# Optimization experiments

Measured on AMD Instinct MI355X. Metric: run time of the kernel, lower is better.

The kernel has to match this reference:

```python
import jax, jax.numpy as jnp
import numpy as np

B, D, L, N, M, K = 256, 512, 196, 1024, 512, 10000  # batch, context, num_ctx, hidden, embed, vocab


def setup_inputs() -> dict:
    key = jax.random.key(0)
    ks = jax.random.split(key, 20)
    r = lambda k, s: jax.random.normal(k, s, dtype=jnp.float32) * 0.02
    return {
        "a_i": jax.random.normal(ks[0], (B, D, L), dtype=jnp.float32),
        "inp": jax.random.normal(ks[1], (B, 1, K), dtype=jnp.float32),
        "hn_prev": jax.random.normal(ks[2], (B, 1, N), dtype=jnp.float32),
        "cn_prev": jax.random.normal(ks[3], (B, 1, N), dtype=jnp.float32),
        "f_att_w": r(ks[4], (N + D,)),  # Linear(n+D -> 1), stored as a vector
        "f_att_b": r(ks[5], (1,)),
        "gate_w": r(ks[6], (N,)),       # Linear(n -> 1)
        "gate_b": r(ks[7], (1,)),
        "E_w": r(ks[8], (M, K)),        # torch Linear weight [out, in]
        "E_b": r(ks[9], (M,)),
        "W_ih": r(ks[10], (4 * N, D + N + M)),  # LSTM input->hidden (i,f,g,o)
        "W_hh": r(ks[11], (4 * N, N)),
        "b_ih": r(ks[12], (4 * N,)),
        "b_hh": r(ks[13], (4 * N,)),
        "Lh_w": r(ks[14], (M, N)),
        "Lh_b": r(ks[15], (M,)),
        "Lz_w": r(ks[16], (M, D)),
        "Lz_b": r(ks[17], (M,)),
        "Lo_w": r(ks[18], (K, M)),
        "Lo_b": r(ks[19], (K,)),
    }


def reference(a_i, inp, hn_prev, cn_prev,
              f_att_w, f_att_b, gate_w, gate_b,
              E_w, E_b, W_ih, W_hh, b_ih, b_hh,
              Lh_w, Lh_b, Lz_w, Lz_b, Lo_w, Lo_b):
    h = hn_prev[:, 0]  # [B, N]
    c = cn_prev[:, 0]  # [B, N]
    # --- additive attention: the 196-iteration torch loop batched into one einsum ---
    # cat((a_i[:,:,i], h)) @ f_att_w splits into the a-part and h-part of the weight.
    w_a, w_h = f_att_w[:D], f_att_w[D:]
    e = jnp.einsum('bdl,d->bl', a_i, w_a) + (h @ w_h)[:, None] + f_att_b  # [B, L]
    alpha = jax.nn.softmax(e, axis=1)                                     # [B, L]
    beta = jax.nn.sigmoid(h @ gate_w + gate_b)                            # [B]
    z = beta[:, None] * jnp.einsum('bl,bdl->bd', alpha, a_i)              # [B, D]
    # --- word embedding ---
    w_emb = inp[:, 0] @ E_w.T + E_b                                       # [B, M]
    # --- single-step LSTM (PyTorch gate order i, f, g, o) ---
    x = jnp.concatenate([w_emb, h, z], axis=1)                            # [B, M+N+D]
    gates = x @ W_ih.T + b_ih + h @ W_hh.T + b_hh                         # [B, 4N]
    i_g, f_g, g_g, o_g = jnp.split(gates, 4, axis=1)
    cn = jax.nn.sigmoid(f_g) * c + jax.nn.sigmoid(i_g) * jnp.tanh(g_g)
    hn = jax.nn.sigmoid(o_g) * jnp.tanh(cn)
    # --- output projection ---
    deep_out = w_emb + (hn @ Lh_w.T + Lh_b) + (z @ Lz_w.T + Lz_b)         # [B, M]
    p_yt = deep_out @ Lo_w.T + Lo_b                                       # [B, K]
    return (p_yt[:, None, :], hn[:, None, :], cn[:, None, :], alpha[:, None, :])
```

## Files before the change

kernel.cpp:

```cpp
#include <hip/hip_runtime.h>
#include <hip/hip_bf16.h>
#include <math.h>

#define BB 256
#define DD 512
#define LL 196
#define NN 1024
#define MM 512
#define KK 10000

#define OUT_PY 0
#define OUT_HN ((size_t)2560000)
#define OUT_CN ((size_t)2822144)
#define OUT_AL ((size_t)3084288)

#define OFF_PE    ((size_t)0)
#define OFF_BETA  ((size_t)401408)
#define OFF_Z     ((size_t)401664)
#define OFF_EMB   ((size_t)532736)
#define OFF_DEEP  ((size_t)663808)
#define OFF_EMBP  ((size_t)794880)
#define OFF_GATESP ((size_t)2892032)
#define OFF_DP    ((size_t)9183488)

typedef __attribute__((ext_vector_type(8))) short short8v;
typedef __attribute__((ext_vector_type(4))) float f32x4;

__device__ __forceinline__ short bfs(float f) {
    __hip_bfloat16 h = __float2bfloat16(f);
    return *reinterpret_cast<short*>(&h);
}

__device__ __forceinline__ short8v stage8(const float* __restrict__ p, bool ok,
                                          int kbase, int Ktot) {
    short8v v;
    if (ok && (kbase + 7 < Ktot)) {
        const float4 x = *(const float4*)(p + kbase);
        const float4 y = *(const float4*)(p + kbase + 4);
        v[0] = bfs(x.x); v[1] = bfs(x.y); v[2] = bfs(x.z); v[3] = bfs(x.w);
        v[4] = bfs(y.x); v[5] = bfs(y.y); v[6] = bfs(y.z); v[7] = bfs(y.w);
    } else {
#pragma unroll
        for (int i = 0; i < 8; ++i) {
            const int k = kbase + i;
            v[i] = bfs((ok && k < Ktot) ? p[k] : 0.f);
        }
    }
    return v;
}

struct GSrc { const float* A; int lda; const float* B; int ldb; int ktn; int K; };

__device__ __forceinline__ void gemm_body(
    const int bx, const int by, const int bz, const int rowBlocks,
    const GSrc s1, const GSrc s2,
    float* __restrict__ C, const int ldc, const int Ncols,
    const int ktPerSplit, const float* __restrict__ bias,
    short (*As)[64][72], short (*Bs)[64][72])
{
    const int t = threadIdx.x;
    const int row0 = bx * 64;
    const int col0 = by * 64;
    const int ktTot = s1.ktn + s2.ktn;
    const int kt0 = bz * ktPerSplit;
    const int nk = min(ktTot, kt0 + ktPerSplit) - kt0;

    const int sr = t >> 2;
    const int sk = (t & 3) << 4;
    const int bc = col0 + sr;
    const bool bok = (bc < Ncols);
    const float* aP1 = s1.A + (size_t)(row0 + sr) * s1.lda;
    const float* bP1 = s1.B + (size_t)(bok ? bc : 0) * s1.ldb;
    const float* aP2 = s2.A ? (s2.A + (size_t)(row0 + sr) * s2.lda) : aP1;
    const float* bP2 = s2.A ? (s2.B + (size_t)(bok ? bc : 0) * s2.ldb) : bP1;

    const int l = t & 63, w = t >> 6;
    const int wrow = (w >> 1) * 32, wcol = (w & 1) * 32;
    const int lr = l & 15, g = l >> 4, g8 = g * 8;

    f32x4 acc[2][2] = {};

    short8v sa0, sa1, sb0, sb1;
    {
        const int ktg = kt0;
        const float* aR; const float* bR; int kk, Kt;
        if (ktg < s1.ktn) { aR = aP1; bR = bP1; kk = (ktg << 6) + sk; Kt = s1.K; }
        else              { aR = aP2; bR = bP2; kk = ((ktg - s1.ktn) << 6) + sk; Kt = s2.K; }
        sa0 = stage8(aR, true, kk, Kt);  sa1 = stage8(aR, true, kk + 8, Kt);
        sb0 = stage8(bR, bok,  kk, Kt);  sb1 = stage8(bR, bok,  kk + 8, Kt);
    }
    *(short8v*)&As[0][sr][sk] = sa0; *(short8v*)&As[0][sr][sk + 8] = sa1;
    *(short8v*)&Bs[0][sr][sk] = sb0; *(short8v*)&Bs[0][sr][sk + 8] = sb1;
    __syncthreads();

    int cur = 0;
    for (int kt = 0; kt < nk; ++kt) {
        const bool more = (kt + 1 < nk);
        if (more) {
            const int ktg = kt0 + kt + 1;
            const float* aR; const float* bR; int kk, Kt;
            if (ktg < s1.ktn) { aR = aP1; bR = bP1; kk = (ktg << 6) + sk; Kt = s1.K; }
            else              { aR = aP2; bR = bP2; kk = ((ktg - s1.ktn) << 6) + sk; Kt = s2.K; }
            sa0 = stage8(aR, true, kk, Kt);  sa1 = stage8(aR, true, kk + 8, Kt);
            sb0 = stage8(bR, bok,  kk, Kt);  sb1 = stage8(bR, bok,  kk + 8, Kt);
        }
#pragma unroll
        for (int ks = 0; ks < 2; ++ks) {
            const int ko = ks * 32 + g8;
            short8v a0 = *(const short8v*)&As[cur][wrow + lr][ko];
            short8v a1 = *(const short8v*)&As[cur][wrow + 16 + lr][ko];
            short8v b0 = *(const short8v*)&Bs[cur][wcol + lr][ko];
            short8v b1 = *(const short8v*)&Bs[cur][wcol + 16 + lr][ko];
            acc[0][0] = __builtin_amdgcn_mfma_f32_16x16x32_bf16(a0, b0, acc[0][0], 0, 0, 0);
            acc[0][1] = __builtin_amdgcn_mfma_f32_16x16x32_bf16(a0, b1, acc[0][1], 0, 0, 0);
            acc[1][0] = __builtin_amdgcn_mfma_f32_16x16x32_bf16(a1, b0, acc[1][0], 0, 0, 0);
            acc[1][1] = __builtin_amdgcn_mfma_f32_16x16x32_bf16(a1, b1, acc[1][1], 0, 0, 0);
        }
        if (more) {
            *(short8v*)&As[cur ^ 1][sr][sk] = sa0;
            *(short8v*)&As[cur ^ 1][sr][sk + 8] = sa1;
            *(short8v*)&Bs[cur ^ 1][sr][sk] = sb0;
            *(short8v*)&Bs[cur ^ 1][sr][sk + 8] = sb1;
        }
        __syncthreads();
        cur ^= 1;
    }

    float* Cp = C + (size_t)bz * ((size_t)rowBlocks * 64) * ldc;
#pragma unroll
    for (int m = 0; m < 2; ++m)
#pragma unroll
        for (int n = 0; n < 2; ++n)
#pragma unroll
            for (int j = 0; j < 4; ++j) {
                const int r = row0 + wrow + m * 16 + g * 4 + j;
                const int c = col0 + wcol + n * 16 + lr;
                if (c < Ncols) {
                    float v = acc[m][n][j];
                    if (bias) v += bias[c];
                    Cp[(size_t)r * ldc + c] = v;
                }
            }
}

__global__ __launch_bounds__(256) void p1_atte_emb(
    const float* __restrict__ a_i, const float* __restrict__ f_att_w,
    float* __restrict__ pe,
    const float* __restrict__ inp, const float* __restrict__ E_w,
    float* __restrict__ embp)
{
    __shared__ __align__(16) short As[2][64][72];
    __shared__ __align__(16) short Bs[2][64][72];
    const int bid = blockIdx.x;
    if (bid < 2048) {
        const int b = bid >> 3, ch = bid & 7;
        const int l = threadIdx.x;
        if (l >= LL) return;
        const float* ap = a_i + ((size_t)b * DD + ch * 64) * LL + l;
        const float* wp = f_att_w + ch * 64;
        float s = 0.f;
#pragma unroll 16
        for (int d = 0; d < 64; ++d) s += ap[(size_t)d * LL] * wp[d];
        pe[((size_t)b * 8 + ch) * LL + l] = s;
    } else {
        const int i = bid - 2048;
        GSrc s1 = {inp, KK, E_w, KK, 157, KK};
        GSrc s2 = {nullptr, 0, nullptr, 0, 0, 0};
        gemm_body(i & 3, (i >> 2) & 7, i >> 5, 4, s1, s2,
                  embp, MM, MM, 10, nullptr, As, Bs);
    }
}

__global__ __launch_bounds__(256) void p2_softmax_embred(
    const float* __restrict__ pe, const float* __restrict__ h,
    const float* __restrict__ f_att_w, const float* __restrict__ f_att_b,
    const float* __restrict__ gate_w, const float* __restrict__ gate_b,
    float* __restrict__ alpha_out, float* __restrict__ beta,
    const float* __restrict__ embp, const float* __restrict__ E_b,
    float* __restrict__ emb)
{
    const int bid = blockIdx.x;
    const int t = threadIdx.x;
    if (bid < 256) {
        const int b = bid;
        __shared__ float red[256];
        __shared__ float red2[256];
        const float4 h4 = *(const float4*)(h + (size_t)b * NN + t * 4);
        const float4 w4 = *(const float4*)(f_att_w + DD + t * 4);
        const float4 g4 = *(const float4*)(gate_w + t * 4);
        float hd = h4.x * w4.x + h4.y * w4.y + h4.z * w4.z + h4.w * w4.w;
        float gd = h4.x * g4.x + h4.y * g4.y + h4.z * g4.z + h4.w * g4.w;
        red[t] = hd; red2[t] = gd;
        __syncthreads();
        for (int s = 128; s > 0; s >>= 1) {
            if (t < s) { red[t] += red[t + s]; red2[t] += red2[t + s]; }
            __syncthreads();
        }
        const float hdot = red[0];
        const float gdot = red2[0];
        __syncthreads();
        float e = -3.4e38f;
        if (t < LL) {
            const float* p = pe + (size_t)b * 8 * LL + t;
            e = hdot + f_att_b[0];
#pragma unroll
            for (int ch = 0; ch < 8; ++ch) e += p[ch * LL];
        }
        red[t] = e;
        __syncthreads();
        for (int s = 128; s > 0; s >>= 1) {
            if (t < s) red[t] = fmaxf(red[t], red[t + s]);
            __syncthreads();
        }
        const float mx = red[0];
        __syncthreads();
        const float ex = (t < LL) ? expf(e - mx) : 0.f;
        red[t] = ex;
        __syncthreads();
        for (int s = 128; s > 0; s >>= 1) {
            if (t < s) red[t] += red[t + s];
            __syncthreads();
        }
        const float inv = 1.f / red[0];
        if (t < LL) alpha_out[(size_t)b * LL + t] = ex * inv;
        if (t == 0) beta[b] = 1.f / (1.f + expf(-(gdot + gate_b[0])));
    } else {
        const int idx = (bid - 256) * 256 + t;
        const int j = idx & 511;
        float v = E_b[j];
#pragma unroll
        for (int s = 0; s < 16; ++s) v += embp[(size_t)s * (BB * 512) + idx];
        emb[idx] = v;
    }
}

__global__ __launch_bounds__(256) void p3_attz_gatesh(
    const float* __restrict__ a_i, const float* __restrict__ alpha,
    const float* __restrict__ beta, float* __restrict__ z,
    const float* __restrict__ h, const float* __restrict__ W_ih,
    const float* __restrict__ W_hh, float* __restrict__ gatesp)
{
    __shared__ __align__(16) short As[2][64][72];
    __shared__ __align__(16) short Bs[2][64][72];
    const int bid = blockIdx.x;
    if (bid < 8192) {
        const int b = bid >> 5, chunk = bid & 31;
        const int wave = threadIdx.x >> 6, lane = threadIdx.x & 63;
        const float* alp = alpha + (size_t)b * LL;
#pragma unroll
        for (int i = 0; i < 4; ++i) {
            const int d = chunk * 16 + wave * 4 + i;
            const float* ap = a_i + ((size_t)b * DD + d) * LL;
            float s = 0.f;
#pragma unroll
            for (int q = 0; q < 4; ++q) {
                const int lidx = lane + q * 64;
                if (lidx < LL) s += ap[lidx] * alp[lidx];
            }
#pragma unroll
            for (int off = 32; off > 0; off >>= 1) s += __shfl_down(s, off, 64);
            if (lane == 0) z[(size_t)b * DD + d] = beta[b] * s;
        }
    } else {
        const int i = bid - 8192;
        GSrc s1 = {h, NN, W_ih + 512, 2048, 16, NN};
        GSrc s2 = {h, NN, W_hh, NN, 16, NN};
        gemm_body(i & 3, (i >> 2) & 63, i >> 8, 4, s1, s2,
                  gatesp, 4096, 4096, 8, nullptr, As, Bs);
    }
}

__global__ __launch_bounds__(256) void p4_gatesez_lz(
    const float* __restrict__ emb, const float* __restrict__ z,
    const float* __restrict__ W_ih, float* __restrict__ gatesp_hi,
    const float* __restrict__ Lz_w, float* __restrict__ dp)
{
    __shared__ __align__(16) short As[2][64][72];
    __shared__ __align__(16) short Bs[2][64][72];
    const int bid = blockIdx.x;
    if (bid < 512) {
        GSrc s1 = {emb, MM, W_ih, 2048, 8, MM};
        GSrc s2 = {z, DD, W_ih + 1536, 2048, 8, DD};
        gemm_body(bid & 3, (bid >> 2) & 63, bid >> 8, 4, s1, s2,
                  gatesp_hi, 4096, 4096, 8, nullptr, As, Bs);
    } else {
        const int i = bid - 512;
        GSrc s1 = {z, DD, Lz_w, DD, 8, DD};
        GSrc s2 = {nullptr, 0, nullptr, 0, 0, 0};
        gemm_body(i & 3, (i >> 2) & 7, i >> 5, 4, s1, s2,
                  dp, MM, MM, 1, nullptr, As, Bs);
    }
}

__global__ __launch_bounds__(256) void p5_lstm(
    const float* __restrict__ gatesp,
    const float* __restrict__ b_ih, const float* __restrict__ b_hh,
    const float* __restrict__ c_prev, float* __restrict__ hn, float* __restrict__ cn)
{
    const int idx = blockIdx.x * 256 + threadIdx.x;
    const int b = idx >> 10, n = idx & 1023;
    float g[4];
#pragma unroll
    for (int gi = 0; gi < 4; ++gi) {
        const int col = gi * 1024 + n;
        const size_t o = (size_t)b * 4096 + col;
        float v = b_ih[col] + b_hh[col];
#pragma unroll
        for (int s = 0; s < 6; ++s) v += gatesp[(size_t)s * (BB * 4096) + o];
        g[gi] = v;
    }
    const float si = 1.f / (1.f + expf(-g[0]));
    const float sf = 1.f / (1.f + expf(-g[1]));
    const float so = 1.f / (1.f + expf(-g[3]));
    const float tg = tanhf(g[2]);
    const float c = c_prev[idx];
    const float cnv = sf * c + si * tg;
    const float hnv = so * tanhf(cnv);
    cn[idx] = cnv;
    hn[idx] = hnv;
}

__global__ __launch_bounds__(256) void p6_lh(
    const float* __restrict__ hn, const float* __restrict__ Lh_w,
    float* __restrict__ dp_hi)
{
    __shared__ __align__(16) short As[2][64][72];
    __shared__ __align__(16) short Bs[2][64][72];
    const int bid = blockIdx.x;
    GSrc s1 = {hn, NN, Lh_w, NN, 16, NN};
    GSrc s2 = {nullptr, 0, nullptr, 0, 0, 0};
    gemm_body(bid & 3, (bid >> 2) & 7, bid >> 5, 4, s1, s2,
              dp_hi, MM, MM, 1, nullptr, As, Bs);
}

__global__ __launch_bounds__(256) void p7_deep(
    const float* __restrict__ emb, const float* __restrict__ dp,
    const float* __restrict__ Lh_b, const float* __restrict__ Lz_b,
    float* __restrict__ deep)
{
    const int idx = blockIdx.x * 256 + threadIdx.x;
    const int j = idx & 511;
    float v = emb[idx] + Lh_b[j] + Lz_b[j];
#pragma unroll
    for (int s = 0; s < 24; ++s) v += dp[(size_t)s * (BB * 512) + idx];
    deep[idx] = v;
}

__global__ __launch_bounds__(256) void p8_pyt(
    const float* __restrict__ deep, const float* __restrict__ Lo_w,
    const float* __restrict__ Lo_b, float* __restrict__ out)
{
    __shared__ __align__(16) short As[2][64][72];
    __shared__ __align__(16) short Bs[2][64][72];
    const int bid = blockIdx.x;
    GSrc s1 = {deep, MM, Lo_w, MM, 8, MM};
    GSrc s2 = {nullptr, 0, nullptr, 0, 0, 0};
    gemm_body(bid & 3, bid >> 2, 0, 4, s1, s2,
              out, KK, KK, 8, Lo_b, As, Bs);
}

extern "C" void kernel_launch(void* const* d_in, const int* in_sizes, int n_in,
                              void* d_out, int out_size, void* d_ws, size_t ws_size,
                              hipStream_t stream)
{
    const float* a_i     = (const float*)d_in[0];
    const float* inp     = (const float*)d_in[1];
    const float* hn_prev = (const float*)d_in[2];
    const float* cn_prev = (const float*)d_in[3];
    const float* f_att_w = (const float*)d_in[4];
    const float* f_att_b = (const float*)d_in[5];
    const float* gate_w  = (const float*)d_in[6];
    const float* gate_b  = (const float*)d_in[7];
    const float* E_w     = (const float*)d_in[8];
    const float* E_b     = (const float*)d_in[9];
    const float* W_ih    = (const float*)d_in[10];
    const float* W_hh    = (const float*)d_in[11];
    const float* b_ih    = (const float*)d_in[12];
    const float* b_hh    = (const float*)d_in[13];
    const float* Lh_w    = (const float*)d_in[14];
    const float* Lh_b    = (const float*)d_in[15];
    const float* Lz_w    = (const float*)d_in[16];
    const float* Lz_b    = (const float*)d_in[17];
    const float* Lo_w    = (const float*)d_in[18];
    const float* Lo_b    = (const float*)d_in[19];

    float* out = (float*)d_out;
    float* ws  = (float*)d_ws;

    float* PE     = ws + OFF_PE;
    float* BETA   = ws + OFF_BETA;
    float* Z      = ws + OFF_Z;
    float* EMB    = ws + OFF_EMB;
    float* DEEP   = ws + OFF_DEEP;
    float* EMBP   = ws + OFF_EMBP;
    float* GATESP = ws + OFF_GATESP;
    float* DP     = ws + OFF_DP;

    p1_atte_emb<<<2560, 256, 0, stream>>>(a_i, f_att_w, PE, inp, E_w, EMBP);

    p2_softmax_embred<<<768, 256, 0, stream>>>(PE, hn_prev, f_att_w, f_att_b,
                                               gate_w, gate_b, out + OUT_AL, BETA,
                                               EMBP, E_b, EMB);

    p3_attz_gatesh<<<9216, 256, 0, stream>>>(a_i, out + OUT_AL, BETA, Z,
                                             hn_prev, W_ih, W_hh, GATESP);

    p4_gatesez_lz<<<768, 256, 0, stream>>>(EMB, Z, W_ih,
                                           GATESP + (size_t)4 * BB * 4096,
                                           Lz_w, DP);

    p5_lstm<<<1024, 256, 0, stream>>>(GATESP, b_ih, b_hh, cn_prev,
                                      out + OUT_HN, out + OUT_CN);

    p6_lh<<<512, 256, 0, stream>>>(out + OUT_HN, Lh_w,
                                   DP + (size_t)8 * BB * 512);

    p7_deep<<<512, 256, 0, stream>>>(EMB, DP, Lh_b, Lz_b, DEEP);

    p8_pyt<<<628, 256, 0, stream>>>(DEEP, Lo_w, Lo_b, out + OUT_PY);
}
```

Measured before the change: 156.9 us.

## Fuse attention softmax and context into one register-resident pass over a_i

The attention score, softmax and context reduction are merged into one block per batch row. That block reads a_i once, packs it to bf16 in registers, transposes it through LDS for the score dot products, then reuses the registers for the alpha-weighted sum. This removes the separate partial-score buffer, the beta buffer and the second full read of a_i. The h-projection GEMM and embedding GEMM are co-scheduled in the same launch, with the embedding split-K halved (20 k-tiles per split), cutting kernel launches from 8 to 7. The cost is heavy register pressure (196 packed values per thread) and bf16 rounding of a_i in the attention math, which may spill or reduce accuracy.

```diff
diff --git a/kernel.cpp b/kernel.cpp
--- a/kernel.cpp
+++ b/kernel.cpp
@@ -14,21 +14,29 @@
 #define OUT_CN ((size_t)2822144)
 #define OUT_AL ((size_t)3084288)
 
-#define OFF_PE    ((size_t)0)
-#define OFF_BETA  ((size_t)401408)
-#define OFF_Z     ((size_t)401664)
-#define OFF_EMB   ((size_t)532736)
-#define OFF_DEEP  ((size_t)663808)
-#define OFF_EMBP  ((size_t)794880)
-#define OFF_GATESP ((size_t)2892032)
-#define OFF_DP    ((size_t)9183488)
+#define OFF_Z      ((size_t)0)
+#define OFF_EMB    ((size_t)131072)
+#define OFF_DEEP   ((size_t)262144)
+#define OFF_EMBP   ((size_t)393216)
+#define OFF_GATESP ((size_t)1441792)
+#define OFF_DP     ((size_t)7733248)
 
 typedef __attribute__((ext_vector_type(8))) short short8v;
 typedef __attribute__((ext_vector_type(4))) float f32x4;
 
-__device__ __forceinline__ short bfs(float f) {
-    __hip_bfloat16 h = __float2bfloat16(f);
-    return *reinterpret_cast<short*>(&h);
+__device__ __forceinline__ unsigned short f2bf(float f) {
+    unsigned int u = __builtin_bit_cast(unsigned int, f);
+    u += 0x7fffu + ((u >> 16) & 1u);
+    return (unsigned short)(u >> 16);
+}
+__device__ __forceinline__ unsigned int pk2(float a, float b) {
+    return ((unsigned int)f2bf(b) << 16) | (unsigned int)f2bf(a);
+}
+__device__ __forceinline__ float bflo(unsigned int u) {
+    return __builtin_bit_cast(float, u << 16);
+}
+__device__ __forceinline__ float bfhi(unsigned int u) {
+    return __builtin_bit_cast(float, u & 0xffff0000u);
 }
 
 __device__ __forceinline__ short8v stage8(const float* __restrict__ p, bool ok,
@@ -37,13 +45,15 @@
     if (ok && (kbase + 7 < Ktot)) {
         const float4 x = *(const float4*)(p + kbase);
         const float4 y = *(const float4*)(p + kbase + 4);
-        v[0] = bfs(x.x); v[1] = bfs(x.y); v[2] = bfs(x.z); v[3] = bfs(x.w);
-        v[4] = bfs(y.x); v[5] = bfs(y.y); v[6] = bfs(y.z); v[7] = bfs(y.w);
+        v[0] = (short)f2bf(x.x); v[1] = (short)f2bf(x.y);
+        v[2] = (short)f2bf(x.z); v[3] = (short)f2bf(x.w);
+        v[4] = (short)f2bf(y.x); v[5] = (short)f2bf(y.y);
+        v[6] = (short)f2bf(y.z); v[7] = (short)f2bf(y.w);
     } else {
 #pragma unroll
         for (int i = 0; i < 8; ++i) {
             const int k = kbase + i;
-            v[i] = bfs((ok && k < Ktot) ? p[k] : 0.f);
+            v[i] = (short)f2bf((ok && k < Ktot) ? p[k] : 0.f);
         }
     }
     return v;
@@ -143,126 +153,144 @@
             }
 }
 
-__global__ __launch_bounds__(256) void p1_atte_emb(
-    const float* __restrict__ a_i, const float* __restrict__ f_att_w,
-    float* __restrict__ pe,
-    const float* __restrict__ inp, const float* __restrict__ E_w,
-    float* __restrict__ embp)
-{
-    __shared__ __align__(16) short As[2][64][72];
-    __shared__ __align__(16) short Bs[2][64][72];
-    const int bid = blockIdx.x;
-    if (bid < 2048) {
-        const int b = bid >> 3, ch = bid & 7;
-        const int l = threadIdx.x;
-        if (l >= LL) return;
-        const float* ap = a_i + ((size_t)b * DD + ch * 64) * LL + l;
-        const float* wp = f_att_w + ch * 64;
-        float s = 0.f;
-#pragma unroll 16
-        for (int d = 0; d < 64; ++d) s += ap[(size_t)d * LL] * wp[d];
-        pe[((size_t)b * 8 + ch) * LL + l] = s;
-    } else {
-        const int i = bid - 2048;
-        GSrc s1 = {inp, KK, E_w, KK, 157, KK};
-        GSrc s2 = {nullptr, 0, nullptr, 0, 0, 0};
-        gemm_body(i & 3, (i >> 2) & 7, i >> 5, 4, s1, s2,
-                  embp, MM, MM, 10, nullptr, As, Bs);
-    }
-}
-
-__global__ __launch_bounds__(256) void p2_softmax_embred(
-    const float* __restrict__ pe, const float* __restrict__ h,
+__global__ __launch_bounds__(256, 2) void k1_att_emb_gatesh(
+    const float* __restrict__ a_i, const float* __restrict__ h,
     const float* __restrict__ f_att_w, const float* __restrict__ f_att_b,
     const float* __restrict__ gate_w, const float* __restrict__ gate_b,
-    float* __restrict__ alpha_out, float* __restrict__ beta,
-    const float* __restrict__ embp, const float* __restrict__ E_b,
-    float* __restrict__ emb)
-{
+    float* __restrict__ alpha_out, float* __restrict__ z,
+    const float* __restrict__ inp, const float* __restrict__ E_w,
+    float* __restrict__ embp,
+    const float* __restrict__ W_ih, const float* __restrict__ W_hh,
+    float* __restrict__ gatesp)
+{
+    __shared__ __align__(16) unsigned char smem[36864];
     const int bid = blockIdx.x;
     const int t = threadIdx.x;
+
     if (bid < 256) {
+        unsigned int* chunk = (unsigned int*)smem;
+        float* wsh = (float*)(smem + 26112);
+        float* al  = wsh + 512;
+        float* red = al + 200;
+        float* sc2 = red + 32;
+        const int lane = t & 63, w = t >> 6;
         const int b = bid;
-        __shared__ float red[256];
-        __shared__ float red2[256];
+
+        wsh[t] = f_att_w[t];
+        wsh[t + 256] = f_att_w[t + 256];
+
         const float4 h4 = *(const float4*)(h + (size_t)b * NN + t * 4);
         const float4 w4 = *(const float4*)(f_att_w + DD + t * 4);
         const float4 g4 = *(const float4*)(gate_w + t * 4);
         float hd = h4.x * w4.x + h4.y * w4.y + h4.z * w4.z + h4.w * w4.w;
         float gd = h4.x * g4.x + h4.y * g4.y + h4.z * g4.z + h4.w * g4.w;
-        red[t] = hd; red2[t] = gd;
-        __syncthreads();
-        for (int s = 128; s > 0; s >>= 1) {
-            if (t < s) { red[t] += red[t + s]; red2[t] += red2[t + s]; }
+#pragma unroll
+        for (int off = 32; off > 0; off >>= 1) {
+            hd += __shfl_down(hd, off, 64);
+            gd += __shfl_down(gd, off, 64);
+        }
+        if (lane == 0) { red[w] = hd; red[16 + w] = gd; }
+
+        unsigned int r0[98], r1[98];
+        const float* p0 = a_i + ((size_t)b * DD + t) * LL;
+        const float* p1 = p0 + (size_t)256 * LL;
+#pragma unroll
+        for (int j = 0; j < 49; ++j) {
+            const float4 v = *(const float4*)(p0 + j * 4);
+            r0[2 * j]     = pk2(v.x, v.y);
+            r0[2 * j + 1] = pk2(v.z, v.w);
+        }
+#pragma unroll
+        for (int j = 0; j < 49; ++j) {
+            const float4 v = *(const float4*)(p1 + j * 4);
+            r1[2 * j]     = pk2(v.x, v.y);
+            r1[2 * j + 1] = pk2(v.z, v.w);
+        }
+        __syncthreads();
+        if (t == 0) {
+            sc2[0] = red[0] + red[1] + red[2] + red[3];
+            sc2[1] = red[16] + red[17] + red[18] + red[19];
+        }
+
+        float e_acc = 0.f;
+#pragma unroll
+        for (int c = 0; c < 8; ++c) {
             __syncthreads();
-        }
-        const float hdot = red[0];
-        const float gdot = red2[0];
-        __syncthreads();
-        float e = -3.4e38f;
+            if (w == (c & 3)) {
+                unsigned int* dst = chunk + lane * 102;
+                if (c < 4) {
+#pragma unroll
+                    for (int j = 0; j < 49; ++j) {
+                        uint2 uv; uv.x = r0[2 * j]; uv.y = r0[2 * j + 1];
+                        *(uint2*)(dst + 2 * j) = uv;
+                    }
+                } else {
+#pragma unroll
+                    for (int j = 0; j < 49; ++j) {
+                        uint2 uv; uv.x = r1[2 * j]; uv.y = r1[2 * j + 1];
+                        *(uint2*)(dst + 2 * j) = uv;
+                    }
+                }
+            }
+            __syncthreads();
+            if (t < LL) {
+                const float* wc = wsh + c * 64;
+                const unsigned short* cs = (const unsigned short*)chunk;
+#pragma unroll
+                for (int d = 0; d < 64; ++d) {
+                    const float av = __builtin_bit_cast(
+                        float, (unsigned int)cs[d * 204 + t] << 16);
+                    e_acc += av * wc[d];
+                }
+            }
+        }
+        __syncthreads();
+
+        float e = (t < LL) ? (e_acc + sc2[0] + f_att_b[0]) : -3.4e38f;
+        float m = e;
+#pragma unroll
+        for (int off = 32; off > 0; off >>= 1) m = fmaxf(m, __shfl_down(m, off, 64));
+        if (lane == 0) red[w] = m;
+        __syncthreads();
+        const float mx = fmaxf(fmaxf(red[0], red[1]), fmaxf(red[2], red[3]));
+        const float ex = (t < LL) ? expf(e - mx) : 0.f;
+        float s = ex;
+#pragma unroll
+        for (int off = 32; off > 0; off >>= 1) s += __shfl_down(s, off, 64);
+        if (lane == 0) red[16 + w] = s;
+        __syncthreads();
+        const float inv = 1.f / (red[16] + red[17] + red[18] + red[19]);
         if (t < LL) {
-            const float* p = pe + (size_t)b * 8 * LL + t;
-            e = hdot + f_att_b[0];
-#pragma unroll
-            for (int ch = 0; ch < 8; ++ch) e += p[ch * LL];
-        }
-        red[t] = e;
-        __syncthreads();
-        for (int s = 128; s > 0; s >>= 1) {
-            if (t < s) red[t] = fmaxf(red[t], red[t + s]);
-            __syncthreads();
-        }
-        const float mx = red[0];
-        __syncthreads();
-        const float ex = (t < LL) ? expf(e - mx) : 0.f;
-        red[t] = ex;
-        __syncthreads();
-        for (int s = 128; s > 0; s >>= 1) {
-            if (t < s) red[t] += red[t + s];
-            __syncthreads();
-        }
-        const float inv = 1.f / red[0];
-        if (t < LL) alpha_out[(size_t)b * LL + t] = ex * inv;
-        if (t == 0) beta[b] = 1.f / (1.f + expf(-(gdot + gate_b[0])));
+            const float a = ex * inv;
+            al[t] = a;
+            alpha_out[(size_t)b * LL + t] = a;
+        }
+        __syncthreads();
+
+        float d0 = 0.f, d1 = 0.f;
+#pragma unroll
+        for (int j = 0; j < 49; ++j) {
+            const float4 a4 = *(const float4*)(al + 4 * j);
+            d0 += bflo(r0[2 * j]) * a4.x + bfhi(r0[2 * j]) * a4.y
+                + bflo(r0[2 * j + 1]) * a4.z + bfhi(r0[2 * j + 1]) * a4.w;
+            d1 += bflo(r1[2 * j]) * a4.x + bfhi(r1[2 * j]) * a4.y
+                + bflo(r1[2 * j + 1]) * a4.z + bfhi(r1[2 * j + 1]) * a4.w;
+        }
+        const float beta = 1.f / (1.f + expf(-(sc2[1] + gate_b[0])));
+        z[(size_t)b * DD + t] = beta * d0;
+        z[(size_t)b * DD + 256 + t] = beta * d1;
+    } else if (bid < 512) {
+        short (*As)[64][72] = (short (*)[64][72])smem;
+        short (*Bs)[64][72] = (short (*)[64][72])(smem + 18432);
+        const int i = bid - 256;
+        GSrc s1 = {inp, KK, E_w, KK, 157, KK};
+        GSrc s2 = {nullptr, 0, nullptr, 0, 0, 0};
+        gemm_body(i & 3, (i >> 2) & 7, i >> 5, 4, s1, s2,
+                  embp, MM, MM, 20, nullptr, As, Bs);
     } else {
-        const int idx = (bid - 256) * 256 + t;
-        const int j = idx & 511;
-        float v = E_b[j];
-#pragma unroll
-        for (int s = 0; s < 16; ++s) v += embp[(size_t)s * (BB * 512) + idx];
-        emb[idx] = v;
-    }
-}
-
-__global__ __launch_bounds__(256) void p3_attz_gatesh(
-    const float* __restrict__ a_i, const float* __restrict__ alpha,
-    const float* __restrict__ beta, float* __restrict__ z,
-    const float* __restrict__ h, const float* __restrict__ W_ih,
-    const float* __restrict__ W_hh, float* __restrict__ gatesp)
-{
-    __shared__ __align__(16) short As[2][64][72];
-    __shared__ __align__(16) short Bs[2][64][72];
-    const int bid = blockIdx.x;
-    if (bid < 8192) {
-        const int b = bid >> 5, chunk = bid & 31;
-        const int wave = threadIdx.x >> 6, lane = threadIdx.x & 63;
-        const float* alp = alpha + (size_t)b * LL;
-#pragma unroll
-        for (int i = 0; i < 4; ++i) {
-            const int d = chunk * 16 + wave * 4 + i;
-            const float* ap = a_i + ((size_t)b * DD + d) * LL;
-            float s = 0.f;
-#pragma unroll
-            for (int q = 0; q < 4; ++q) {
-                const int lidx = lane + q * 64;
-                if (lidx < LL) s += ap[lidx] * alp[lidx];
-            }
-#pragma unroll
-            for (int off = 32; off > 0; off >>= 1) s += __shfl_down(s, off, 64);
-            if (lane == 0) z[(size_t)b * DD + d] = beta[b] * s;
-        }
-    } else {
-        const int i = bid - 8192;
+        short (*As)[64][72] = (short (*)[64][72])smem;
+        short (*Bs)[64][72] = (short (*)[64][72])(smem + 18432);
+        const int i = bid - 512;
         GSrc s1 = {h, NN, W_ih + 512, 2048, 16, NN};
         GSrc s2 = {h, NN, W_hh, NN, 16, NN};
         gemm_body(i & 3, (i >> 2) & 63, i >> 8, 4, s1, s2,
@@ -270,13 +298,26 @@
     }
 }
 
-__global__ __launch_bounds__(256) void p4_gatesez_lz(
+__global__ __launch_bounds__(256) void k2_embred(
+    const float* __restrict__ embp, const float* __restrict__ E_b,
+    float* __restrict__ emb)
+{
+    const int idx = blockIdx.x * 256 + threadIdx.x;
+    const int j = idx & 511;
+    float v = E_b[j];
+#pragma unroll
+    for (int s = 0; s < 8; ++s) v += embp[(size_t)s * (BB * 512) + idx];
+    emb[idx] = v;
+}
+
+__global__ __launch_bounds__(256) void k3_gatesez_lz(
     const float* __restrict__ emb, const float* __restrict__ z,
     const float* __restrict__ W_ih, float* __restrict__ gatesp_hi,
     const float* __restrict__ Lz_w, float* __restrict__ dp)
 {
-    __shared__ __align__(16) short As[2][64][72];
-    __shared__ __align__(16) short Bs[2][64][72];
+    __shared__ __align__(16) unsigned char smem[36864];
+    short (*As)[64][72] = (short (*)[64][72])smem;
+    short (*Bs)[64][72] = (short (*)[64][72])(smem + 18432);
     const int bid = blockIdx.x;
     if (bid < 512) {
         GSrc s1 = {emb, MM, W_ih, 2048, 8, MM};
@@ -292,7 +333,7 @@
     }
 }
 
-__global__ __launch_bounds__(256) void p5_lstm(
+__global__ __launch_bounds__(256) void k4_lstm(
     const float* __restrict__ gatesp,
     const float* __restrict__ b_ih, const float* __restrict__ b_hh,
     const float* __restrict__ c_prev, float* __restrict__ hn, float* __restrict__ cn)
@@ -320,12 +361,13 @@
     hn[idx] = hnv;
 }
 
-__global__ __launch_bounds__(256) void p6_lh(
+__global__ __launch_bounds__(256) void k5_lh(
     const float* __restrict__ hn, const float* __restrict__ Lh_w,
     float* __restrict__ dp_hi)
 {
-    __shared__ __align__(16) short As[2][64][72];
-    __shared__ __align__(16) short Bs[2][64][72];
+    __shared__ __align__(16) unsigned char smem[36864];
+    short (*As)[64][72] = (short (*)[64][72])smem;
+    short (*Bs)[64][72] = (short (*)[64][72])(smem + 18432);
     const int bid = blockIdx.x;
     GSrc s1 = {hn, NN, Lh_w, NN, 16, NN};
     GSrc s2 = {nullptr, 0, nullptr, 0, 0, 0};
@@ -333,7 +375,7 @@
               dp_hi, MM, MM, 1, nullptr, As, Bs);
 }
 
-__global__ __launch_bounds__(256) void p7_deep(
+__global__ __launch_bounds__(256) void k6_deep(
     const float* __restrict__ emb, const float* __restrict__ dp,
     const float* __restrict__ Lh_b, const float* __restrict__ Lz_b,
     float* __restrict__ deep)
@@ -346,12 +388,13 @@
     deep[idx] = v;
 }
 
-__global__ __launch_bounds__(256) void p8_pyt(
+__global__ __launch_bounds__(256) void k7_pyt(
     const float* __restrict__ deep, const float* __restrict__ Lo_w,
     const float* __restrict__ Lo_b, float* __restrict__ out)
 {
-    __shared__ __align__(16) short As[2][64][72];
-    __shared__ __align__(16) short Bs[2][64][72];
+    __shared__ __align__(16) unsigned char smem[36864];
+    short (*As)[64][72] = (short (*)[64][72])smem;
+    short (*Bs)[64][72] = (short (*)[64][72])(smem + 18432);
     const int bid = blockIdx.x;
     GSrc s1 = {deep, MM, Lo_w, MM, 8, MM};
     GSrc s2 = {nullptr, 0, nullptr, 0, 0, 0};
@@ -387,8 +430,6 @@
     float* out = (float*)d_out;
     float* ws  = (float*)d_ws;
 
-    float* PE     = ws + OFF_PE;
-    float* BETA   = ws + OFF_BETA;
     float* Z      = ws + OFF_Z;
     float* EMB    = ws + OFF_EMB;
     float* DEEP   = ws + OFF_DEEP;
@@ -396,26 +437,23 @@
     float* GATESP = ws + OFF_GATESP;
     float* DP     = ws + OFF_DP;
 
-    p1_atte_emb<<<2560, 256, 0, stream>>>(a_i, f_att_w, PE, inp, E_w, EMBP);
-
-    p2_softmax_embred<<<768, 256, 0, stream>>>(PE, hn_prev, f_att_w, f_att_b,
-                                               gate_w, gate_b, out + OUT_AL, BETA,
-                                               EMBP, E_b, EMB);
-
-    p3_attz_gatesh<<<9216, 256, 0, stream>>>(a_i, out + OUT_AL, BETA, Z,
-                                             hn_prev, W_ih, W_hh, GATESP);
-
-    p4_gatesez_lz<<<768, 256, 0, stream>>>(EMB, Z, W_ih,
+    k1_att_emb_gatesh<<<1536, 256, 0, stream>>>(
+        a_i, hn_prev, f_att_w, f_att_b, gate_w, gate_b,
+        out + OUT_AL, Z, inp, E_w, EMBP, W_ih, W_hh, GATESP);
+
+    k2_embred<<<512, 256, 0, stream>>>(EMBP, E_b, EMB);
+
+    k3_gatesez_lz<<<768, 256, 0, stream>>>(EMB, Z, W_ih,
                                            GATESP + (size_t)4 * BB * 4096,
                                            Lz_w, DP);
 
-    p5_lstm<<<1024, 256, 0, stream>>>(GATESP, b_ih, b_hh, cn_prev,
+    k4_lstm<<<1024, 256, 0, stream>>>(GATESP, b_ih, b_hh, cn_prev,
                                       out + OUT_HN, out + OUT_CN);
 
-    p6_lh<<<512, 256, 0, stream>>>(out + OUT_HN, Lh_w,
+    k5_lh<<<512, 256, 0, stream>>>(out + OUT_HN, Lh_w,
                                    DP + (size_t)8 * BB * 512);
 
-    p7_deep<<<512, 256, 0, stream>>>(EMB, DP, Lh_b, Lz_b, DEEP);
-
-    p8_pyt<<<628, 256, 0, stream>>>(DEEP, Lo_w, Lo_b, out + OUT_PY);
-}
+    k6_deep<<<512, 256, 0, stream>>>(EMB, DP, Lh_b, Lz_b, DEEP);
+
+    k7_pyt<<<628, 256, 0, stream>>>(DEEP, Lo_w, Lo_b, out + OUT_PY);
+}
```

New measurement: 241.5 us. 1.54x slower.

## Rebalance kernel stages and vectorize attention reductions over a_i

Applied to the files above, without the earlier changes.

The h-dependent gate GEMM moves from the third launch into the first, where it runs alongside the attention-energy and embedding work. The embedding-dependent gate GEMM now runs with the z-reduction launch, leaving only the z part for the fourth kernel. The attention energy and context reductions are rewritten to use float4 loads over L with per-wave register buffering, and split-K counts are retuned (embedding 8 partials, gates 8 partials). It also adds a manual round-to-nearest-even bf16 conversion and shares one shared-memory pool across the different branch kinds.

```diff
diff --git a/kernel.cpp b/kernel.cpp
--- a/kernel.cpp
+++ b/kernel.cpp
@@ -14,21 +14,22 @@
 #define OUT_CN ((size_t)2822144)
 #define OUT_AL ((size_t)3084288)
 
-#define OFF_PE    ((size_t)0)
-#define OFF_BETA  ((size_t)401408)
-#define OFF_Z     ((size_t)401664)
-#define OFF_EMB   ((size_t)532736)
-#define OFF_DEEP  ((size_t)663808)
-#define OFF_EMBP  ((size_t)794880)
-#define OFF_GATESP ((size_t)2892032)
-#define OFF_DP    ((size_t)9183488)
+#define OFF_PE     ((size_t)0)
+#define OFF_BETA   ((size_t)802816)
+#define OFF_Z      ((size_t)803072)
+#define OFF_EMB    ((size_t)934144)
+#define OFF_DEEP   ((size_t)1065216)
+#define OFF_EMBP   ((size_t)1196288)
+#define OFF_GATESP ((size_t)2244864)
+#define OFF_DP     ((size_t)10633472)
 
 typedef __attribute__((ext_vector_type(8))) short short8v;
 typedef __attribute__((ext_vector_type(4))) float f32x4;
 
-__device__ __forceinline__ short bfs(float f) {
-    __hip_bfloat16 h = __float2bfloat16(f);
-    return *reinterpret_cast<short*>(&h);
+__device__ __forceinline__ unsigned short f2bf(float f) {
+    unsigned int u = __builtin_bit_cast(unsigned int, f);
+    u += 0x7fffu + ((u >> 16) & 1u);
+    return (unsigned short)(u >> 16);
 }
 
 __device__ __forceinline__ short8v stage8(const float* __restrict__ p, bool ok,
@@ -37,13 +38,15 @@
     if (ok && (kbase + 7 < Ktot)) {
         const float4 x = *(const float4*)(p + kbase);
         const float4 y = *(const float4*)(p + kbase + 4);
-        v[0] = bfs(x.x); v[1] = bfs(x.y); v[2] = bfs(x.z); v[3] = bfs(x.w);
-        v[4] = bfs(y.x); v[5] = bfs(y.y); v[6] = bfs(y.z); v[7] = bfs(y.w);
+        v[0] = (short)f2bf(x.x); v[1] = (short)f2bf(x.y);
+        v[2] = (short)f2bf(x.z); v[3] = (short)f2bf(x.w);
+        v[4] = (short)f2bf(y.x); v[5] = (short)f2bf(y.y);
+        v[6] = (short)f2bf(y.z); v[7] = (short)f2bf(y.w);
     } else {
 #pragma unroll
         for (int i = 0; i < 8; ++i) {
             const int k = kbase + i;
-            v[i] = bfs((ok && k < Ktot) ? p[k] : 0.f);
+            v[i] = (short)f2bf((ok && k < Ktot) ? p[k] : 0.f);
         }
     }
     return v;
@@ -143,35 +146,63 @@
             }
 }
 
-__global__ __launch_bounds__(256) void p1_atte_emb(
+__global__ __launch_bounds__(256) void k1_atte_emb_gatesh(
     const float* __restrict__ a_i, const float* __restrict__ f_att_w,
     float* __restrict__ pe,
     const float* __restrict__ inp, const float* __restrict__ E_w,
-    float* __restrict__ embp)
-{
-    __shared__ __align__(16) short As[2][64][72];
-    __shared__ __align__(16) short Bs[2][64][72];
-    const int bid = blockIdx.x;
-    if (bid < 2048) {
-        const int b = bid >> 3, ch = bid & 7;
-        const int l = threadIdx.x;
-        if (l >= LL) return;
-        const float* ap = a_i + ((size_t)b * DD + ch * 64) * LL + l;
-        const float* wp = f_att_w + ch * 64;
-        float s = 0.f;
-#pragma unroll 16
-        for (int d = 0; d < 64; ++d) s += ap[(size_t)d * LL] * wp[d];
-        pe[((size_t)b * 8 + ch) * LL + l] = s;
-    } else {
-        const int i = bid - 2048;
+    float* __restrict__ embp,
+    const float* __restrict__ h, const float* __restrict__ W_ih,
+    const float* __restrict__ W_hh, float* __restrict__ gatesp)
+{
+    __shared__ __align__(16) unsigned char smem[36864];
+    const int bid = blockIdx.x;
+    const int t = threadIdx.x;
+
+    if (bid < 4096) {
+        float* pw = (float*)smem;
+        const int b = bid >> 4, ch = bid & 15;
+        const int w = t >> 6, lane = t & 63;
+        const int d0 = ch * 32 + w * 8;
+        const float* base = a_i + ((size_t)b * DD + d0) * LL;
+        float e4[4] = {0.f, 0.f, 0.f, 0.f};
+        if (lane < 49) {
+            float4 rbuf[8];
+#pragma unroll
+            for (int i = 0; i < 8; ++i)
+                rbuf[i] = *(const float4*)(base + (size_t)i * LL + lane * 4);
+#pragma unroll
+            for (int i = 0; i < 8; ++i) {
+                const float wa = f_att_w[d0 + i];
+                e4[0] += rbuf[i].x * wa; e4[1] += rbuf[i].y * wa;
+                e4[2] += rbuf[i].z * wa; e4[3] += rbuf[i].w * wa;
+            }
+            *(float4*)&pw[w * 200 + lane * 4] = *(const float4*)e4;
+        }
+        __syncthreads();
+        if (t < LL) {
+            const float s = pw[t] + pw[200 + t] + pw[400 + t] + pw[600 + t];
+            pe[((size_t)b * 16 + ch) * LL + t] = s;
+        }
+    } else if (bid < 4352) {
+        short (*As)[64][72] = (short (*)[64][72])smem;
+        short (*Bs)[64][72] = (short (*)[64][72])(smem + 18432);
+        const int i = bid - 4096;
         GSrc s1 = {inp, KK, E_w, KK, 157, KK};
         GSrc s2 = {nullptr, 0, nullptr, 0, 0, 0};
         gemm_body(i & 3, (i >> 2) & 7, i >> 5, 4, s1, s2,
-                  embp, MM, MM, 10, nullptr, As, Bs);
-    }
-}
-
-__global__ __launch_bounds__(256) void p2_softmax_embred(
+                  embp, MM, MM, 20, nullptr, As, Bs);
+    } else {
+        short (*As)[64][72] = (short (*)[64][72])smem;
+        short (*Bs)[64][72] = (short (*)[64][72])(smem + 18432);
+        const int i = bid - 4352;
+        GSrc s1 = {h, NN, W_ih + 512, 2048, 16, NN};
+        GSrc s2 = {h, NN, W_hh, NN, 16, NN};
+        gemm_body(i & 3, (i >> 2) & 63, i >> 8, 4, s1, s2,
+                  gatesp, 4096, 4096, 8, nullptr, As, Bs);
+    }
+}
+
+__global__ __launch_bounds__(256) void k2_softmax_embred(
     const float* __restrict__ pe, const float* __restrict__ h,
     const float* __restrict__ f_att_w, const float* __restrict__ f_att_b,
     const float* __restrict__ gate_w, const float* __restrict__ gate_b,
@@ -201,10 +232,10 @@
         __syncthreads();
         float e = -3.4e38f;
         if (t < LL) {
-            const float* p = pe + (size_t)b * 8 * LL + t;
+            const float* p = pe + (size_t)b * 16 * LL + t;
             e = hdot + f_att_b[0];
 #pragma unroll
-            for (int ch = 0; ch < 8; ++ch) e += p[ch * LL];
+            for (int ch = 0; ch < 16; ++ch) e += p[ch * LL];
         }
         red[t] = e;
         __syncthreads();
@@ -229,60 +260,71 @@
         const int j = idx & 511;
         float v = E_b[j];
 #pragma unroll
-        for (int s = 0; s < 16; ++s) v += embp[(size_t)s * (BB * 512) + idx];
+        for (int s = 0; s < 8; ++s) v += embp[(size_t)s * (BB * 512) + idx];
         emb[idx] = v;
     }
 }
 
-__global__ __launch_bounds__(256) void p3_attz_gatesh(
+__global__ __launch_bounds__(256) void k3_attz_gatese(
     const float* __restrict__ a_i, const float* __restrict__ alpha,
     const float* __restrict__ beta, float* __restrict__ z,
-    const float* __restrict__ h, const float* __restrict__ W_ih,
-    const float* __restrict__ W_hh, float* __restrict__ gatesp)
-{
-    __shared__ __align__(16) short As[2][64][72];
-    __shared__ __align__(16) short Bs[2][64][72];
-    const int bid = blockIdx.x;
-    if (bid < 8192) {
-        const int b = bid >> 5, chunk = bid & 31;
-        const int wave = threadIdx.x >> 6, lane = threadIdx.x & 63;
-        const float* alp = alpha + (size_t)b * LL;
-#pragma unroll
-        for (int i = 0; i < 4; ++i) {
-            const int d = chunk * 16 + wave * 4 + i;
-            const float* ap = a_i + ((size_t)b * DD + d) * LL;
-            float s = 0.f;
-#pragma unroll
-            for (int q = 0; q < 4; ++q) {
-                const int lidx = lane + q * 64;
-                if (lidx < LL) s += ap[lidx] * alp[lidx];
-            }
+    const float* __restrict__ emb, const float* __restrict__ W_ih,
+    float* __restrict__ gatesp_e)
+{
+    __shared__ __align__(16) unsigned char smem[36864];
+    const int bid = blockIdx.x;
+    const int t = threadIdx.x;
+
+    if (bid < 4096) {
+        float* al = (float*)smem;
+        const int b = bid >> 4, ch = bid & 15;
+        const int w = t >> 6, lane = t & 63;
+        if (t < LL) al[t] = alpha[(size_t)b * LL + t];
+        __syncthreads();
+        const int d0 = ch * 32 + w * 8;
+        const float* base = a_i + ((size_t)b * DD + d0) * LL;
+        const float bet = beta[b];
+        float4 av = make_float4(0.f, 0.f, 0.f, 0.f);
+        float4 rbuf[8];
+        if (lane < 49) {
+            av = *(const float4*)&al[lane * 4];
+#pragma unroll
+            for (int i = 0; i < 8; ++i)
+                rbuf[i] = *(const float4*)(base + (size_t)i * LL + lane * 4);
+        }
+#pragma unroll
+        for (int i = 0; i < 8; ++i) {
+            float s = (lane < 49) ? (rbuf[i].x * av.x + rbuf[i].y * av.y +
+                                     rbuf[i].z * av.z + rbuf[i].w * av.w) : 0.f;
 #pragma unroll
             for (int off = 32; off > 0; off >>= 1) s += __shfl_down(s, off, 64);
-            if (lane == 0) z[(size_t)b * DD + d] = beta[b] * s;
+            if (lane == 0) z[(size_t)b * DD + d0 + i] = bet * s;
         }
     } else {
-        const int i = bid - 8192;
-        GSrc s1 = {h, NN, W_ih + 512, 2048, 16, NN};
-        GSrc s2 = {h, NN, W_hh, NN, 16, NN};
+        short (*As)[64][72] = (short (*)[64][72])smem;
+        short (*Bs)[64][72] = (short (*)[64][72])(smem + 18432);
+        const int i = bid - 4096;
+        GSrc s1 = {emb, MM, W_ih, 2048, 8, MM};
+        GSrc s2 = {nullptr, 0, nullptr, 0, 0, 0};
         gemm_body(i & 3, (i >> 2) & 63, i >> 8, 4, s1, s2,
-                  gatesp, 4096, 4096, 8, nullptr, As, Bs);
-    }
-}
-
-__global__ __launch_bounds__(256) void p4_gatesez_lz(
-    const float* __restrict__ emb, const float* __restrict__ z,
-    const float* __restrict__ W_ih, float* __restrict__ gatesp_hi,
+                  gatesp_e, 4096, 4096, 4, nullptr, As, Bs);
+    }
+}
+
+__global__ __launch_bounds__(256) void k4_gatesz_lz(
+    const float* __restrict__ z, const float* __restrict__ W_ih,
+    float* __restrict__ gatesp_z,
     const float* __restrict__ Lz_w, float* __restrict__ dp)
 {
-    __shared__ __align__(16) short As[2][64][72];
-    __shared__ __align__(16) short Bs[2][64][72];
+    __shared__ __align__(16) unsigned char smem[36864];
+    short (*As)[64][72] = (short (*)[64][72])smem;
+    short (*Bs)[64][72] = (short (*)[64][72])(smem + 18432);
     const int bid = blockIdx.x;
     if (bid < 512) {
-        GSrc s1 = {emb, MM, W_ih, 2048, 8, MM};
-        GSrc s2 = {z, DD, W_ih + 1536, 2048, 8, DD};
+        GSrc s1 = {z, DD, W_ih + 1536, 2048, 8, DD};
+        GSrc s2 = {nullptr, 0, nullptr, 0, 0, 0};
         gemm_body(bid & 3, (bid >> 2) & 63, bid >> 8, 4, s1, s2,
-                  gatesp_hi, 4096, 4096, 8, nullptr, As, Bs);
+                  gatesp_z, 4096, 4096, 4, nullptr, As, Bs);
     } else {
         const int i = bid - 512;
         GSrc s1 = {z, DD, Lz_w, DD, 8, DD};
@@ -292,7 +334,7 @@
     }
 }
 
-__global__ __launch_bounds__(256) void p5_lstm(
+__global__ __launch_bounds__(256) void k5_lstm(
     const float* __restrict__ gatesp,
     const float* __restrict__ b_ih, const float* __restrict__ b_hh,
     const float* __restrict__ c_prev, float* __restrict__ hn, float* __restrict__ cn)
@@ -306,7 +348,7 @@
         const size_t o = (size_t)b * 4096 + col;
         float v = b_ih[col] + b_hh[col];
 #pragma unroll
-        for (int s = 0; s < 6; ++s) v += gatesp[(size_t)s * (BB * 4096) + o];
+        for (int s = 0; s < 8; ++s) v += gatesp[(size_t)s * (BB * 4096) + o];
         g[gi] = v;
     }
     const float si = 1.f / (1.f + expf(-g[0]));
@@ -320,12 +362,13 @@
     hn[idx] = hnv;
 }
 
-__global__ __launch_bounds__(256) void p6_lh(
+__global__ __launch_bounds__(256) void k6_lh(
     const float* __restrict__ hn, const float* __restrict__ Lh_w,
     float* __restrict__ dp_hi)
 {
-    __shared__ __align__(16) short As[2][64][72];
-    __shared__ __align__(16) short Bs[2][64][72];
+    __shared__ __align__(16) unsigned char smem[36864];
+    short (*As)[64][72] = (short (*)[64][72])smem;
+    short (*Bs)[64][72] = (short (*)[64][72])(smem + 18432);
     const int bid = blockIdx.x;
     GSrc s1 = {hn, NN, Lh_w, NN, 16, NN};
     GSrc s2 = {nullptr, 0, nullptr, 0, 0, 0};
@@ -333,7 +376,7 @@
               dp_hi, MM, MM, 1, nullptr, As, Bs);
 }
 
-__global__ __launch_bounds__(256) void p7_deep(
+__global__ __launch_bounds__(256) void k7_deep(
     const float* __restrict__ emb, const float* __restrict__ dp,
     const float* __restrict__ Lh_b, const float* __restrict__ Lz_b,
     float* __restrict__ deep)
@@ -346,12 +389,13 @@
     deep[idx] = v;
 }
 
-__global__ __launch_bounds__(256) void p8_pyt(
+__global__ __launch_bounds__(256) void k8_pyt(
     const float* __restrict__ deep, const float* __restrict__ Lo_w,
     const float* __restrict__ Lo_b, float* __restrict__ out)
 {
-    __shared__ __align__(16) short As[2][64][72];
-    __shared__ __align__(16) short Bs[2][64][72];
+    __shared__ __align__(16) unsigned char smem[36864];
+    short (*As)[64][72] = (short (*)[64][72])smem;
+    short (*Bs)[64][72] = (short (*)[64][72])(smem + 18432);
     const int bid = blockIdx.x;
     GSrc s1 = {deep, MM, Lo_w, MM, 8, MM};
     GSrc s2 = {nullptr, 0, nullptr, 0, 0, 0};
@@ -396,26 +440,28 @@
     float* GATESP = ws + OFF_GATESP;
     float* DP     = ws + OFF_DP;
 
-    p1_atte_emb<<<2560, 256, 0, stream>>>(a_i, f_att_w, PE, inp, E_w, EMBP);
-
-    p2_softmax_embred<<<768, 256, 0, stream>>>(PE, hn_prev, f_att_w, f_att_b,
+    k1_atte_emb_gatesh<<<5376, 256, 0, stream>>>(
+        a_i, f_att_w, PE, inp, E_w, EMBP, hn_prev, W_ih, W_hh, GATESP);
+
+    k2_softmax_embred<<<768, 256, 0, stream>>>(PE, hn_prev, f_att_w, f_att_b,
                                                gate_w, gate_b, out + OUT_AL, BETA,
                                                EMBP, E_b, EMB);
 
-    p3_attz_gatesh<<<9216, 256, 0, stream>>>(a_i, out + OUT_AL, BETA, Z,
-                                             hn_prev, W_ih, W_hh, GATESP);
-
-    p4_gatesez_lz<<<768, 256, 0, stream>>>(EMB, Z, W_ih,
-                                           GATESP + (size_t)4 * BB * 4096,
-                                           Lz_w, DP);
-
-    p5_lstm<<<1024, 256, 0, stream>>>(GATESP, b_ih, b_hh, cn_prev,
+    k3_attz_gatese<<<4608, 256, 0, stream>>>(a_i, out + OUT_AL, BETA, Z,
+                                             EMB, W_ih,
+                                             GATESP + (size_t)4 * BB * 4096);
+
+    k4_gatesz_lz<<<768, 256, 0, stream>>>(Z, W_ih,
+                                          GATESP + (size_t)6 * BB * 4096,
+                                          Lz_w, DP);
+
+    k5_lstm<<<1024, 256, 0, stream>>>(GATESP, b_ih, b_hh, cn_prev,
                                       out + OUT_HN, out + OUT_CN);
 
-    p6_lh<<<512, 256, 0, stream>>>(out + OUT_HN, Lh_w,
+    k6_lh<<<512, 256, 0, stream>>>(out + OUT_HN, Lh_w,
                                    DP + (size_t)8 * BB * 512);
 
-    p7_deep<<<512, 256, 0, stream>>>(EMB, DP, Lh_b, Lz_b, DEEP);
-
-    p8_pyt<<<628, 256, 0, stream>>>(DEEP, Lo_w, Lo_b, out + OUT_PY);
-}
+    k7_deep<<<512, 256, 0, stream>>>(EMB, DP, Lh_b, Lz_b, DEEP);
+
+    k8_pyt<<<628, 256, 0, stream>>>(DEEP, Lo_w, Lo_b, out + OUT_PY);
+}
```

New measurement: 156.3 us. About the same (-0.4%).
